# Optimization experiments

Measured on AMD Instinct MI355X. Metric: run time of the kernel, lower is better.

The kernel has to match this reference:

```python
import jax, jax.numpy as jnp
import numpy as np

B, N, D = 8, 1024, 256
H = 8
DH = D // H
R = 4          # relation types 0..3; adj value 4 = no relation
FF = 1024
EPS = 1e-5


def _lin(k, fan_in, shape):
    return jax.random.normal(k, shape, jnp.float32) * (1.0 / np.sqrt(fan_in))


def setup_inputs() -> dict:
    key = jax.random.key(0)
    ks = jax.random.split(key, 16)
    src = jax.random.normal(ks[0], (B, N, D), jnp.float32)
    adj_matrix = jax.random.randint(ks[1], (B, N, N), 0, 5, dtype=jnp.int32)
    Wq = _lin(ks[2], D, (D, D)); bq = jnp.zeros((D,), jnp.float32)
    Wk = _lin(ks[3], D, (D, D)); bk = jnp.zeros((D,), jnp.float32)
    Wv = _lin(ks[4], D, (R, D, D)); bv = jnp.zeros((R, D), jnp.float32)
    Wo = _lin(ks[5], D, (D, D)); bo = jnp.zeros((D,), jnp.float32)
    W1 = _lin(ks[6], D, (D, FF)); b1 = jnp.zeros((FF,), jnp.float32)
    W2 = _lin(ks[7], FF, (FF, D)); b2 = jnp.zeros((D,), jnp.float32)
    g1 = jnp.ones((D,), jnp.float32); beta1 = jnp.zeros((D,), jnp.float32)
    g2 = jnp.ones((D,), jnp.float32); beta2 = jnp.zeros((D,), jnp.float32)
    return dict(src=src, adj_matrix=adj_matrix, Wq=Wq, bq=bq, Wk=Wk, bk=bk,
                Wv=Wv, bv=bv, Wo=Wo, bo=bo, W1=W1, b1=b1, W2=W2, b2=b2,
                g1=g1, beta1=beta1, g2=g2, beta2=beta2)


def _ln(x, g, b):
    m = x.mean(-1, keepdims=True)
    v = ((x - m) ** 2).mean(-1, keepdims=True)
    return (x - m) * jax.lax.rsqrt(v + EPS) * g + b


def reference(src, adj_matrix, Wq, bq, Wk, bk, Wv, bv, Wo, bo, W1, b1, W2, b2, g1, beta1, g2, beta2):
    Bb, Nn, Dm = src.shape
    h, dh = H, Dm // H
    q = (src @ Wq + bq).reshape(Bb, Nn, h, dh).transpose(0, 2, 1, 3)  # (B,H,N,dh)
    k = (src @ Wk + bk).reshape(Bb, Nn, h, dh).transpose(0, 2, 1, 3)
    scores = jnp.einsum('bhid,bhjd->bhij', q, k) / np.sqrt(dh)
    attn = jax.nn.softmax(scores, axis=-1)                             # (B,H,N,N)
    out = jnp.zeros_like(q)
    for r in range(Wv.shape[0]):  # small fixed relation loop, matches module
        v_r = (src @ Wv[r] + bv[r]).reshape(Bb, Nn, h, dh).transpose(0, 2, 1, 3)
        mask = (adj_matrix == r)[:, None]                              # (B,1,N,N)
        out = out + jnp.einsum('bhij,bhjd->bhid', attn * mask, v_r)
    attn_out = out.transpose(0, 2, 1, 3).reshape(Bb, Nn, Dm) @ Wo + bo
    x = _ln(src + attn_out, g1, beta1)
    ff = jax.nn.gelu(x @ W1 + b1, approximate=False) @ W2 + b2
    return _ln(x + ff, g2, beta2)
```

## Files before the change

### kernel.cpp

```cpp
#include <hip/hip_runtime.h>
#include <hip/hip_bf16.h>
#include <cmath>

constexpr int CB  = 8;
constexpr int CN  = 1024;
constexpr int CD  = 256;
constexpr int CH  = 8;
constexpr int CDH = 32;
constexpr int CR  = 4;
constexpr int CFF = 1024;
constexpr float CEPS = 1e-5f;
constexpr float CS = 0.25503480f;
constexpr size_t SZH = (size_t)CB * CH * CN * CDH;

#define MODE_QK    0
#define MODE_FFN1  2
#define MODE_VT    4

typedef float v4f __attribute__((ext_vector_type(4)));
typedef short v8s __attribute__((ext_vector_type(8)));

static __device__ __forceinline__ short f2bf(float f) {
    unsigned u = __builtin_bit_cast(unsigned, f);
    u += 0x7fff + ((u >> 16) & 1);
    return (short)(u >> 16);
}
static __device__ __forceinline__ float bf2f(short s) {
    unsigned u = ((unsigned)(unsigned short)s) << 16;
    return __builtin_bit_cast(float, u);
}
static __device__ __forceinline__ unsigned cvtpk_bf16(float lo, float hi) {
    unsigned r;
    asm("v_cvt_pk_bf16_f32 %0, %1, %2" : "=v"(r) : "v"(lo), "v"(hi));
    return r;
}

static __device__ __forceinline__ void async_copy16(const void* g, void* l) {
    __builtin_amdgcn_global_load_lds(
        (const __attribute__((address_space(1))) void*)g,
        (__attribute__((address_space(3))) void*)l, 16, 0, 0);
}

template<int BM, int BN, int MODE>
__device__ __forceinline__ void gemm_body(
    const short* __restrict__ A, const short* __restrict__ Bw,
    const float* __restrict__ biasv, void* __restrict__ dest,
    int M, int K, int Nw, int bx, int by, short* smem)
{
    constexpr int WTM = BM / 2, WTN = BN / 2;
    constexpr int TM = WTM / 16, TN = WTN / 16;
    short* As = smem;
    short* Bs = smem + 2 * BM * 32;

    const int t    = threadIdx.x;
    const int lane = t & 63;
    const int w    = t >> 6;
    const int quad = lane >> 4, l15 = lane & 15;
    const int wm = w >> 1, wn = w & 1;
    const int m0 = bx * BM, n0 = by * BN;

    const int srow = lane >> 2;
    const int scol = (lane & 3) * 8;

    v4f acc[TM][TN];
    #pragma unroll
    for (int i = 0; i < TM; ++i)
        #pragma unroll
        for (int j = 0; j < TN; ++j) acc[i][j] = (v4f){0.f, 0.f, 0.f, 0.f};

    const int NK = K >> 5;

    auto stage = [&](int buf, int kt) {
        #pragma unroll
        for (int u = 0; u < BM / 64; ++u) {
            const int e0 = (w * (BM / 64) + u) * 512;
            const int row = (e0 >> 5) + srow;
            async_copy16(A + (size_t)(m0 + row) * K + kt + scol,
                         &As[buf * BM * 32 + e0]);
        }
        #pragma unroll
        for (int u = 0; u < BN / 64; ++u) {
            const int e0 = (w * (BN / 64) + u) * 512;
            const int row = (e0 >> 5) + srow;
            async_copy16(Bw + (size_t)(n0 + row) * K + kt + scol,
                         &Bs[buf * BN * 32 + e0]);
        }
    };

    stage(0, 0);

    for (int it = 0; it < NK; ++it) {
        __syncthreads();
        if (it + 1 < NK) stage((it + 1) & 1, (it + 1) << 5);

        const int buf = it & 1;
        v8s af[TM], bfr[TN];
        #pragma unroll
        for (int i = 0; i < TM; ++i)
            af[i] = *(const v8s*)&As[buf * BM * 32 +
                                     (wm * WTM + i * 16 + l15) * 32 + quad * 8];
        #pragma unroll
        for (int j = 0; j < TN; ++j)
            bfr[j] = *(const v8s*)&Bs[buf * BN * 32 +
                                      (wn * WTN + j * 16 + l15) * 32 + quad * 8];
        #pragma unroll
        for (int i = 0; i < TM; ++i)
            #pragma unroll
            for (int j = 0; j < TN; ++j)
                acc[i][j] = __builtin_amdgcn_mfma_f32_16x16x32_bf16(
                    af[i], bfr[j], acc[i][j], 0, 0, 0);
    }

    #pragma unroll
    for (int i = 0; i < TM; ++i) {
        #pragma unroll
        for (int j = 0; j < TN; ++j) {
            const int mb = m0 + wm * WTM + i * 16 + quad * 4;
            const int n  = n0 + wn * WTN + j * 16 + l15;
            float vals[4];
            if (MODE == MODE_VT) {
                #pragma unroll
                for (int rr = 0; rr < 4; ++rr) vals[rr] = acc[i][j][rr] + biasv[mb + rr];
            } else {
                #pragma unroll
                for (int rr = 0; rr < 4; ++rr) vals[rr] = acc[i][j][rr] + biasv[n];
            }

            if (MODE == MODE_QK) {
                if (n0 < 256) {
                    #pragma unroll
                    for (int rr = 0; rr < 4; ++rr) vals[rr] *= CS;
                }
                const int b = mb >> 10, ii0 = mb & 1023;
                const int plane = n >> 8, nn = n & 255;
                const int h = nn >> 5, d = nn & 31;
                #pragma unroll
                for (int rr = 0; rr < 4; ++rr)
                    ((short*)dest)[(size_t)plane * SZH +
                        (((size_t)(b * CH + h)) * CN + ii0 + rr) * CDH + d] =
                        f2bf(vals[rr]);
            } else if (MODE == MODE_VT) {
                const int b = n >> 10, ii = n & 1023;
                const int iip = (ii & ~63) | ((ii & 15) << 2) | ((ii >> 4) & 3);
                #pragma unroll
                for (int rr = 0; rr < 4; ++rr) {
                    const int m = mb + rr;
                    const int r2 = m >> 8, hd = m & 255;
                    const int h = hd >> 5, d = hd & 31;
                    ((short*)dest)[2 * SZH +
                        (((size_t)(r2 * 64 + b * CH + h)) * CDH + d) * CN + iip] =
                        f2bf(vals[rr]);
                }
            } else {
                #pragma unroll
                for (int rr = 0; rr < 4; ++rr) {
                    const size_t idx = (size_t)(mb + rr) * Nw + n;
                    const float xx = vals[rr];
                    const float E = exp2f(2.302217f * (xx + 0.044715f * xx * xx * xx));
                    ((short*)dest)[idx] = f2bf(xx * E / (E + 1.f));
                }
            }
        }
    }
}

template<int BM, int BN, int MODE>
__global__ __launch_bounds__(256)
void gemm_mfma(const short* __restrict__ A, const short* __restrict__ Bw,
               const float* __restrict__ biasv, void* __restrict__ dest,
               int M, int K, int Nw)
{
    extern __shared__ short smem[];
    gemm_body<BM, BN, MODE>(A, Bw, biasv, dest, M, K, Nw,
                            blockIdx.x, blockIdx.y, smem);
}

__global__ __launch_bounds__(256)
void proj_kernel(const short* __restrict__ src_bf, const short* __restrict__ wqkvT,
                 const float* __restrict__ bpack, short* __restrict__ qkv,
                 const int* __restrict__ adj, unsigned char* __restrict__ adj4)
{
    extern __shared__ short smem[];
    const int g = blockIdx.x;
    if (g < 512) {
        gemm_body<64, 128, MODE_QK>(src_bf, wqkvT, bpack, qkv,
                                    8192, 256, 512, g >> 2, g & 3, smem);
    } else if (g < 1536) {
        const int h2 = g - 512;
        gemm_body<64, 128, MODE_VT>(wqkvT + 512 * 256, src_bf, bpack + 512,
                                    qkv, 1024, 256, 8192, h2 & 15, h2 >> 4, smem);
    } else {
        const int nout = CB * CN * CN / 8;
        for (int i = (g - 1536) * 256 + threadIdx.x; i < nout; i += 512 * 256) {
            const int m   = i & 7;
            const int T   = (i >> 3) & 15;
            const int row = i >> 7;
            const int* p = adj + (size_t)row * CN + T * 64 + 2 * m;
            const int2 q0 = *(const int2*)(p);
            const int2 q1 = *(const int2*)(p + 16);
            const int2 q2 = *(const int2*)(p + 32);
            const int2 q3 = *(const int2*)(p + 48);
            const unsigned pk =
                (unsigned)(q0.x & 0xf)         | ((unsigned)(q1.x & 0xf) << 4)  |
                ((unsigned)(q2.x & 0xf) << 8)  | ((unsigned)(q3.x & 0xf) << 12) |
                ((unsigned)(q0.y & 0xf) << 16) | ((unsigned)(q1.y & 0xf) << 20) |
                ((unsigned)(q2.y & 0xf) << 24) | ((unsigned)(q3.y & 0xf) << 28);
            ((unsigned*)adj4)[i] = pk;
        }
    }
}

template<bool OUTF, bool OUTB, bool ADDBF>
__global__ __launch_bounds__(256)
void gemm_ln32(const short* __restrict__ A, const short* __restrict__ Bw,
               const float* __restrict__ biasv, const void* __restrict__ addp,
               const float* __restrict__ gw, const float* __restrict__ be,
               float* __restrict__ outf, short* __restrict__ outb, int K)
{
    __shared__ short As[2][16 * 32];
    __shared__ short Bs[2][256 * 32];
    __shared__ float redS[16][4], redQ[16][4];

    const int t    = threadIdx.x;
    const int lane = t & 63;
    const int w    = t >> 6;
    const int quad = lane >> 4, l15 = lane & 15;
    const int m0   = blockIdx.x * 16;

    const int srow = lane >> 2;
    const int scol = (lane & 3) * 8;

    v4f acc[4];
    #pragma unroll
    for (int j = 0; j < 4; ++j) acc[j] = (v4f){0.f, 0.f, 0.f, 0.f};

    const int NK = K >> 5;

    auto stage = [&](int buf, int kt) {
        if (t < 64)
            async_copy16(A + (size_t)(m0 + (t >> 2)) * K + kt + (t & 3) * 8,
                         &As[buf][t * 8]);
        #pragma unroll
        for (int u = 0; u < 4; ++u) {
            const int e0 = (w * 4 + u) * 512;
            async_copy16(Bw + (size_t)((e0 >> 5) + srow) * K + kt + scol,
                         &Bs[buf][e0]);
        }
    };

    stage(0, 0);

    for (int it = 0; it < NK; ++it) {
        __syncthreads();
        if (it + 1 < NK) stage((it + 1) & 1, (it + 1) << 5);

        const int buf = it & 1;
        const v8s af = *(const v8s*)&As[buf][l15 * 32 + quad * 8];
        #pragma unroll
        for (int j = 0; j < 4; ++j) {
            const v8s bfr = *(const v8s*)&Bs[buf][(w * 64 + 16 * j + l15) * 32 + quad * 8];
            acc[j] = __builtin_amdgcn_mfma_f32_16x16x32_bf16(af, bfr, acc[j], 0, 0, 0);
        }
    }

    float v[4][4];
    #pragma unroll
    for (int rr = 0; rr < 4; ++rr) {
        const int row = m0 + quad * 4 + rr;
        float s = 0.f, sq = 0.f;
        #pragma unroll
        for (int j = 0; j < 4; ++j) {
            const int n = w * 64 + 16 * j + l15;
            const size_t idx = (size_t)row * CD + n;
            const float addv = ADDBF ? bf2f(((const short*)addp)[idx])
                                     : ((const float*)addp)[idx];
            const float x = acc[j][rr] + biasv[n] + addv;
            v[rr][j] = x;
            s += x; sq += x * x;
        }
        #pragma unroll
        for (int off = 1; off < 16; off <<= 1) {
            s  += __shfl_xor(s, off);
            sq += __shfl_xor(sq, off);
        }
        if (l15 == 0) {
            redS[quad * 4 + rr][w] = s;
            redQ[quad * 4 + rr][w] = sq;
        }
    }
    __syncthreads();

    #pragma unroll
    for (int rr = 0; rr < 4; ++rr) {
        const int r16 = quad * 4 + rr;
        const int row = m0 + r16;
        const float s  = (redS[r16][0] + redS[r16][1]) + (redS[r16][2] + redS[r16][3]);
        const float sq = (redQ[r16][0] + redQ[r16][1]) + (redQ[r16][2] + redQ[r16][3]);
        const float mean = s * (1.f / CD);
        const float var  = sq * (1.f / CD) - mean * mean;
        const float rstd = rsqrtf(var + CEPS);
        #pragma unroll
        for (int j = 0; j < 4; ++j) {
            const int n = w * 64 + 16 * j + l15;
            const float y = (v[rr][j] - mean) * rstd * gw[n] + be[n];
            if (OUTF) outf[(size_t)row * CD + n] = y;
            if (OUTB) outb[(size_t)row * CD + n] = f2bf(y);
        }
    }
}

__global__ __launch_bounds__(256)
void prep(const float* __restrict__ src,
          const float* __restrict__ Wq, const float* __restrict__ Wk,
          const float* __restrict__ Wv, const float* __restrict__ Wo,
          const float* __restrict__ W1, const float* __restrict__ W2,
          const float* __restrict__ bq, const float* __restrict__ bk,
          const float* __restrict__ bv, const float* __restrict__ bo,
          const float* __restrict__ b1, const float* __restrict__ b2,
          short* __restrict__ src_bf,
          short* __restrict__ wqkvT, short* __restrict__ woT,
          short* __restrict__ w1T, short* __restrict__ w2T,
          float* __restrict__ bpack)
{
    __shared__ float tile[64][65];
    const int bx = blockIdx.x, t = threadIdx.x;
    if (bx < 2048) {
        const int i = bx * 256 + t;
        const float4 v = ((const float4*)src)[i];
        short4 o;
        o.x = f2bf(v.x); o.y = f2bf(v.y); o.z = f2bf(v.z); o.w = f2bf(v.w);
        ((short4*)src_bf)[i] = o;
    } else if (bx < 2288) {
        const int tt = bx - 2048;
        const float* S; short* D;
        int Sstride, Dstride, k0, srccol, dstrow;
        if (tt < 96) {
            const int tk = tt & 3, tn = tt >> 2;
            const int ng = tn * 64;
            Sstride = 256; Dstride = 256; k0 = tk * 64;
            dstrow = tn * 64; D = wqkvT;
            if (ng < 256)      { S = Wq; srccol = ng; }
            else if (ng < 512) { S = Wk; srccol = ng - 256; }
            else { const int r = (ng - 512) >> 8;
                   S = Wv + (size_t)r * 65536; srccol = (ng - 512) & 255; }
        } else if (tt < 112) {
            const int u = tt - 96, tk = u & 3, tn = u >> 2;
            S = Wo; Sstride = 256; D = woT; Dstride = 256;
            k0 = tk * 64; srccol = tn * 64; dstrow = tn * 64;
        } else if (tt < 176) {
            const int u = tt - 112, tk = u & 3, tn = u >> 2;
            S = W1; Sstride = 1024; D = w1T; Dstride = 256;
            k0 = tk * 64; srccol = tn * 64; dstrow = tn * 64;
        } else {
            const int u = tt - 176, tk = u & 15, tn = u >> 4;
            S = W2; Sstride = 256; D = w2T; Dstride = 1024;
            k0 = tk * 64; srccol = tn * 64; dstrow = tn * 64;
        }
        #pragma unroll
        for (int u2 = 0; u2 < 4; ++u2) {
            const int kl = (t >> 4) + u2 * 16;
            const int nl = (t & 15) * 4;
            const float4 v = *(const float4*)&S[(size_t)(k0 + kl) * Sstride + srccol + nl];
            tile[kl][nl + 0] = v.x; tile[kl][nl + 1] = v.y;
            tile[kl][nl + 2] = v.z; tile[kl][nl + 3] = v.w;
        }
        __syncthreads();
        #pragma unroll
        for (int u2 = 0; u2 < 4; ++u2) {
            const int nl = (t >> 4) + u2 * 16;
            const int kl = (t & 15) * 4;
            short4 o;
            o.x = f2bf(tile[kl + 0][nl]); o.y = f2bf(tile[kl + 1][nl]);
            o.z = f2bf(tile[kl + 2][nl]); o.w = f2bf(tile[kl + 3][nl]);
            *(short4*)&D[(size_t)(dstrow + nl) * Dstride + k0 + kl] = o;
        }
    } else {
        const int idx = (bx - 2288) * 256 + t;
        float bvv;
        if (idx < 256)       bvv = bq[idx];
        else if (idx < 512)  bvv = bk[idx - 256];
        else if (idx < 1536) bvv = bv[idx - 512];
        else if (idx < 1792) bvv = bo[idx - 1536];
        else if (idx < 2816) bvv = b1[idx - 1792];
        else                 bvv = b2[idx - 2816];
        bpack[idx] = bvv;
    }
}

__global__ __launch_bounds__(256, 4)
void attn_mfma(const short* __restrict__ qg, const short* __restrict__ kg,
               const short* __restrict__ vt, const unsigned char* __restrict__ adj4,
               short* __restrict__ outh)
{
    __shared__ __align__(16) short vtl[2][8192];
    __shared__ __align__(16) short ps[4096];

    const int t    = threadIdx.x;
    const int lane = t & 63;
    const int w    = t >> 6;
    const int quad = lane >> 4;
    const int l15  = lane & 15;
    const int g    = blockIdx.x;
    const int b    = g & 7;
    const int h    = (g >> 3) & 7;
    const int i0   = (g >> 6) * 64;
    const int bhh  = b * CH + h;
    const size_t bh = (size_t)bhh;

    const v8s qfrag = *(const v8s*)&qg[(bh * CN + i0 + 16 * w + l15) * CDH + quad * 8];

    const short* vsrc[4];
    #pragma unroll
    for (int u = 0; u < 4; ++u) {
        const int gl = t + 256 * u;
        const int r = gl >> 8, d = (gl >> 3) & 31, gc = gl & 7;
        vsrc[u] = vt + ((size_t)(r * 64 + bhh) * CDH + d) * CN + (gc ^ (d & 7)) * 8;
    }
    const short* kbase = kg + (bh * CN + l15) * CDH + quad * 8;
    const unsigned char* abase =
        adj4 + ((size_t)(b * CN) + i0 + 16 * w + l15) * (CN / 2) + quad * 4;

    v4f oacc[2];
    oacc[0] = (v4f){0.f, 0.f, 0.f, 0.f};
    oacc[1] = (v4f){0.f, 0.f, 0.f, 0.f};
    float plsum[4] = {0.f, 0.f, 0.f, 0.f};
    const int arow = 16 * w + l15;
    const int psw  = (l15 & 7) * 8;

    #pragma unroll
    for (int u = 0; u < 4; ++u)
        async_copy16(vsrc[u], &vtl[0][(t + 256 * u) * 8]);
    v8s kpre[4];
    #pragma unroll
    for (int jb = 0; jb < 4; ++jb)
        kpre[jb] = *(const v8s*)(kbase + (16 * jb) * CDH);
    unsigned apre0 = *(const unsigned*)(abase);
    unsigned apre1 = *(const unsigned*)(abase + 16);

    for (int jt = 0; jt < 16; ++jt) {
        __syncthreads();
        const int p = jt & 1;

        v4f sacc[4];
        #pragma unroll
        for (int jb = 0; jb < 4; ++jb)
            sacc[jb] = __builtin_amdgcn_mfma_f32_16x16x32_bf16(
                qfrag, kpre[jb], (v4f){0.f, 0.f, 0.f, 0.f}, 0, 0, 0);

        const unsigned a0 = apre0, a1 = apre1;
        const int jn = (jt + 1) & 15;
        #pragma unroll
        for (int u = 0; u < 4; ++u)
            async_copy16(vsrc[u] + jn * 64, &vtl[p ^ 1][(t + 256 * u) * 8]);
        #pragma unroll
        for (int jb = 0; jb < 4; ++jb)
            kpre[jb] = *(const v8s*)(kbase + (jn * 64 + 16 * jb) * CDH);
        apre0 = *(const unsigned*)(abase + jn * 32);
        apre1 = *(const unsigned*)(abase + jn * 32 + 16);

        #pragma unroll
        for (int rr = 0; rr < 4; ++rr) {
            const int prow = 16 * w + quad * 4 + rr;
            float pv[4];
            #pragma unroll
            for (int jb = 0; jb < 4; ++jb) pv[jb] = exp2f(sacc[jb][rr]);
            plsum[rr] += (pv[0] + pv[1]) + (pv[2] + pv[3]);
            const unsigned lo = cvtpk_bf16(pv[0], pv[1]);
            const unsigned hi = cvtpk_bf16(pv[2], pv[3]);
            const int off = prow * 64 + (((l15 >> 1) ^ (prow & 7)) * 8) + (l15 & 1) * 4;
            *(uint2*)&ps[off] = make_uint2(lo, hi);
        }

        #pragma unroll
        for (int kb = 0; kb < 2; ++kb) {
            const int4 praw = *(const int4*)&ps[arow * 64 + (((4 * kb + quad) * 8) ^ psw)];
            const unsigned ab32 = kb ? a1 : a0;
            const unsigned P[4] = {(unsigned)praw.x, (unsigned)praw.y,
                                   (unsigned)praw.z, (unsigned)praw.w};
            unsigned pf[4][4];
            #pragma unroll
            for (int u = 0; u < 4; ++u) {
                const unsigned sel = 0x0c000c00u | (unsigned)u | ((unsigned)u << 16);
                const unsigned a2 = __builtin_amdgcn_perm(ab32, ab32, sel) & 0x00F0000Fu;
                #pragma unroll
                for (int r = 0; r < 4; ++r) {
                    const unsigned x = a2 ^ ((unsigned)r | ((unsigned)r << 20));
                    unsigned tt, mm;
                    asm("v_pk_add_i16 %0, %1, %2"
                        : "=v"(tt) : "v"(x), "v"(0xffffffffu));
                    asm("v_pk_ashrrev_i16 %0, %1, %2"
                        : "=v"(mm) : "v"(0x000f000fu), "v"(tt));
                    pf[r][u] = P[u] & mm;
                }
            }
            #pragma unroll
            for (int r = 0; r < 4; ++r) {
                const v8s pfr = __builtin_bit_cast(v8s,
                    make_uint4(pf[r][0], pf[r][1], pf[r][2], pf[r][3]));
                #pragma unroll
                for (int cb = 0; cb < 2; ++cb) {
                    const v8s vfrag = *(const v8s*)&vtl[p][r * 2048 +
                        (16 * cb + l15) * 64 + (((4 * kb + quad) * 8) ^ psw)];
                    oacc[cb] = __builtin_amdgcn_mfma_f32_16x16x32_bf16(
                        pfr, vfrag, oacc[cb], 0, 0, 0);
                }
            }
        }
    }

    #pragma unroll
    for (int rr = 0; rr < 4; ++rr) {
        float l = plsum[rr];
        #pragma unroll
        for (int off = 1; off < 16; off <<= 1) l += __shfl_xor(l, off);
        const float inv = 1.f / l;
        const int row = i0 + 16 * w + quad * 4 + rr;
        #pragma unroll
        for (int cb = 0; cb < 2; ++cb)
            outh[((size_t)b * CN + row) * CD + h * CDH + 16 * cb + l15] =
                f2bf(oacc[cb][rr] * inv);
    }
}

extern "C" void kernel_launch(void* const* d_in, const int* in_sizes, int n_in,
                              void* d_out, int out_size, void* d_ws, size_t ws_size,
                              hipStream_t stream)
{
    const float* src = (const float*)d_in[0];
    const int*   adj = (const int*)d_in[1];
    const float* Wq  = (const float*)d_in[2];
    const float* bq  = (const float*)d_in[3];
    const float* Wk  = (const float*)d_in[4];
    const float* bk  = (const float*)d_in[5];
    const float* Wv  = (const float*)d_in[6];
    const float* bv  = (const float*)d_in[7];
    const float* Wo  = (const float*)d_in[8];
    const float* bo  = (const float*)d_in[9];
    const float* W1  = (const float*)d_in[10];
    const float* b1  = (const float*)d_in[11];
    const float* W2  = (const float*)d_in[12];
    const float* b2  = (const float*)d_in[13];
    const float* g1  = (const float*)d_in[14];
    const float* be1 = (const float*)d_in[15];
    const float* g2  = (const float*)d_in[16];
    const float* be2 = (const float*)d_in[17];
    float* out = (float*)d_out;

    char* wsb = (char*)d_ws;
    const size_t MB = (size_t)1 << 20;

    unsigned char* adj4 = (unsigned char*)(wsb);
    short* qkv_bf = (short*)(wsb + 8 * MB);
    short* src_bf = (short*)(wsb + 32 * MB);
    short* wqkvT  = (short*)(wsb + 36 * MB);
    short* woT    = (short*)(wsb + 36 * MB + 768 * 1024);
    short* w1T    = (short*)(wsb + 36 * MB + 896 * 1024);
    short* w2T    = (short*)(wsb + 36 * MB + 1408 * 1024);
    float* bpack  = (float*)(wsb + 36 * MB + 1920 * 1024);
    short* heads_bf = (short*)(wsb + 38 * MB);
    short* x_bf   = (short*)(wsb + 32 * MB);
    short* h1_bf  = (short*)(wsb + 16 * MB);

    const int M = CB * CN;
    dim3 blk(256);

    prep<<<dim3(2300), blk, 0, stream>>>(src, Wq, Wk, Wv, Wo, W1, W2,
        bq, bk, bv, bo, b1, b2, src_bf, wqkvT, woT, w1T, w2T, bpack);

    proj_kernel<<<dim3(2048), blk, 24576, stream>>>(
        src_bf, wqkvT, bpack, qkv_bf, adj, adj4);

    attn_mfma<<<dim3(1024), blk, 0, stream>>>(
        qkv_bf, qkv_bf + SZH, qkv_bf + 2 * SZH, adj4, heads_bf);

    gemm_ln32<false, true, false><<<dim3(M / 16), blk, 0, stream>>>(
        heads_bf, woT, bpack + 1536, src, g1, be1, nullptr, x_bf, CD);

    gemm_mfma<64, 128, MODE_FFN1><<<dim3(M / 64, CFF / 128), blk, 24576, stream>>>(
        x_bf, w1T, bpack + 1792, h1_bf, M, CD, CFF);

    gemm_ln32<true, false, true><<<dim3(M / 16), blk, 0, stream>>>(
        h1_bf, w2T, bpack + 2816, x_bf, g2, be2, out, nullptr, CFF);
}
```

Measured before the change: 229.0 us.

## Compute transposed scores so P feeds PV MFMA from registers, dropping LDS staging

```diff
diff --git a/kernel.cpp b/kernel.cpp
--- a/kernel.cpp
+++ b/kernel.cpp
@@ -41,6 +41,7 @@
         (__attribute__((address_space(3))) void*)l, 16, 0, 0);
 }
 
+
 template<int BM, int BN, int MODE>
 __device__ __forceinline__ void gemm_body(
     const short* __restrict__ A, const short* __restrict__ Bw,
@@ -141,7 +142,10 @@
                         f2bf(vals[rr]);
             } else if (MODE == MODE_VT) {
                 const int b = n >> 10, ii = n & 1023;
-                const int iip = (ii & ~63) | ((ii & 15) << 2) | ((ii >> 4) & 3);
+                const int jj = ii & 63;
+                const int cc = (((jj >> 4) & 1) << 5) | (((jj >> 2) & 3) << 3) |
+                               (((jj >> 5) & 1) << 2) | (jj & 3);
+                const int iip = (ii & ~63) | cc;
                 #pragma unroll
                 for (int rr = 0; rr < 4; ++rr) {
                     const int m = mb + rr;
@@ -192,19 +196,18 @@
     } else {
         const int nout = CB * CN * CN / 8;
         for (int i = (g - 1536) * 256 + threadIdx.x; i < nout; i += 512 * 256) {
-            const int m   = i & 7;
-            const int T   = (i >> 3) & 15;
+            const int dwi = i & 127;
             const int row = i >> 7;
-            const int* p = adj + (size_t)row * CN + T * 64 + 2 * m;
-            const int2 q0 = *(const int2*)(p);
-            const int2 q1 = *(const int2*)(p + 16);
-            const int2 q2 = *(const int2*)(p + 32);
-            const int2 q3 = *(const int2*)(p + 48);
+            const int T   = dwi >> 3, kq = dwi & 7;
+            const int j0  = T * 64 + (kq & 3) * 4 + (kq >> 2) * 16;
+            const int* p = adj + (size_t)row * CN + j0;
+            const int4 q0 = *(const int4*)(p);
+            const int4 q1 = *(const int4*)(p + 32);
             const unsigned pk =
-                (unsigned)(q0.x & 0xf)         | ((unsigned)(q1.x & 0xf) << 4)  |
-                ((unsigned)(q2.x & 0xf) << 8)  | ((unsigned)(q3.x & 0xf) << 12) |
-                ((unsigned)(q0.y & 0xf) << 16) | ((unsigned)(q1.y & 0xf) << 20) |
-                ((unsigned)(q2.y & 0xf) << 24) | ((unsigned)(q3.y & 0xf) << 28);
+                (unsigned)(q0.x & 0xf)         | ((unsigned)(q0.y & 0xf) << 4)  |
+                ((unsigned)(q0.z & 0xf) << 8)  | ((unsigned)(q0.w & 0xf) << 12) |
+                ((unsigned)(q1.x & 0xf) << 16) | ((unsigned)(q1.y & 0xf) << 20) |
+                ((unsigned)(q1.z & 0xf) << 24) | ((unsigned)(q1.w & 0xf) << 28);
             ((unsigned*)adj4)[i] = pk;
         }
     }
@@ -393,7 +396,6 @@
                short* __restrict__ outh)
 {
     __shared__ __align__(16) short vtl[2][8192];
-    __shared__ __align__(16) short ps[4096];
 
     const int t    = threadIdx.x;
     const int lane = t & 63;
@@ -423,9 +425,8 @@
     v4f oacc[2];
     oacc[0] = (v4f){0.f, 0.f, 0.f, 0.f};
     oacc[1] = (v4f){0.f, 0.f, 0.f, 0.f};
-    float plsum[4] = {0.f, 0.f, 0.f, 0.f};
-    const int arow = 16 * w + l15;
-    const int psw  = (l15 & 7) * 8;
+    float plsum = 0.f;
+    const int psw = (l15 & 7) * 8;
 
     #pragma unroll
     for (int u = 0; u < 4; ++u)
@@ -445,7 +446,7 @@
         #pragma unroll
         for (int jb = 0; jb < 4; ++jb)
             sacc[jb] = __builtin_amdgcn_mfma_f32_16x16x32_bf16(
-                qfrag, kpre[jb], (v4f){0.f, 0.f, 0.f, 0.f}, 0, 0, 0);
+                kpre[jb], qfrag, (v4f){0.f, 0.f, 0.f, 0.f}, 0, 0, 0);
 
         const unsigned a0 = apre0, a1 = apre1;
         const int jn = (jt + 1) & 15;
@@ -458,25 +459,24 @@
         apre0 = *(const unsigned*)(abase + jn * 32);
         apre1 = *(const unsigned*)(abase + jn * 32 + 16);
 
-        #pragma unroll
-        for (int rr = 0; rr < 4; ++rr) {
-            const int prow = 16 * w + quad * 4 + rr;
-            float pv[4];
+        float pv[4][4];
+        #pragma unroll
+        for (int jb = 0; jb < 4; ++jb)
             #pragma unroll
-            for (int jb = 0; jb < 4; ++jb) pv[jb] = exp2f(sacc[jb][rr]);
-            plsum[rr] += (pv[0] + pv[1]) + (pv[2] + pv[3]);
-            const unsigned lo = cvtpk_bf16(pv[0], pv[1]);
-            const unsigned hi = cvtpk_bf16(pv[2], pv[3]);
-            const int off = prow * 64 + (((l15 >> 1) ^ (prow & 7)) * 8) + (l15 & 1) * 4;
-            *(uint2*)&ps[off] = make_uint2(lo, hi);
-        }
+            for (int rr = 0; rr < 4; ++rr) pv[jb][rr] = exp2f(sacc[jb][rr]);
+        plsum += ((pv[0][0] + pv[0][1]) + (pv[0][2] + pv[0][3]))
+               + ((pv[1][0] + pv[1][1]) + (pv[1][2] + pv[1][3]))
+               + ((pv[2][0] + pv[2][1]) + (pv[2][2] + pv[2][3]))
+               + ((pv[3][0] + pv[3][1]) + (pv[3][2] + pv[3][3]));
 
         #pragma unroll
         for (int kb = 0; kb < 2; ++kb) {
-            const int4 praw = *(const int4*)&ps[arow * 64 + (((4 * kb + quad) * 8) ^ psw)];
+            const unsigned P[4] = {
+                cvtpk_bf16(pv[kb][0],     pv[kb][1]),
+                cvtpk_bf16(pv[kb][2],     pv[kb][3]),
+                cvtpk_bf16(pv[kb + 2][0], pv[kb + 2][1]),
+                cvtpk_bf16(pv[kb + 2][2], pv[kb + 2][3])};
             const unsigned ab32 = kb ? a1 : a0;
-            const unsigned P[4] = {(unsigned)praw.x, (unsigned)praw.y,
-                                   (unsigned)praw.z, (unsigned)praw.w};
             unsigned pf[4][4];
             #pragma unroll
             for (int u = 0; u < 4; ++u) {
@@ -508,12 +508,12 @@
         }
     }
 
+    float plF = plsum;
+    plF += __shfl_xor(plF, 16);
+    plF += __shfl_xor(plF, 32);
     #pragma unroll
     for (int rr = 0; rr < 4; ++rr) {
-        float l = plsum[rr];
-        #pragma unroll
-        for (int off = 1; off < 16; off <<= 1) l += __shfl_xor(l, off);
-        const float inv = 1.f / l;
+        const float inv = 1.f / __shfl(plF, quad * 4 + rr);
         const int row = i0 + 16 * w + quad * 4 + rr;
         #pragma unroll
         for (int cb = 0; cb < 2; ++cb)
```

New measurement: 228.7 us. About the same (-0.1%).
